# Kernel optimization log

Hardware: AMD Instinct MI355X
Metric: run time of the kernel (lower is better)

The kernel has to match this reference:

```python
import jax, jax.numpy as jnp
import numpy as np

N_CHEM = 200000
N_GENE = 20000
N_EDGES = 1000000
IN, HID, OUT = 128, 256, 128


def _seg_mean(msg, dst, num_segments):
    # DGL fn.mean: mean of incoming messages; nodes with zero in-degree get 0.
    s = jax.ops.segment_sum(msg, dst, num_segments=num_segments)
    cnt = jax.ops.segment_sum(jnp.ones((msg.shape[0],), msg.dtype), dst,
                              num_segments=num_segments)[:, None]
    return jnp.where(cnt > 0, s / jnp.maximum(cnt, 1.0), 0.0)


def setup_inputs() -> dict:
    key = jax.random.key(0)
    ks = jax.random.split(key, 12)
    d = {
        'src_cg': jax.random.randint(ks[0], (N_EDGES,), 0, N_CHEM, dtype=jnp.int32),
        'dst_cg': jax.random.randint(ks[1], (N_EDGES,), 0, N_GENE, dtype=jnp.int32),
        'src_gc': jax.random.randint(ks[2], (N_EDGES,), 0, N_GENE, dtype=jnp.int32),
        'dst_gc': jax.random.randint(ks[3], (N_EDGES,), 0, N_CHEM, dtype=jnp.int32),
        'embed_chem': jax.random.normal(ks[4], (N_CHEM, IN), jnp.float32) * 0.1,
        'embed_gene': jax.random.normal(ks[5], (N_GENE, IN), jnp.float32) * 0.1,
        'W1_cg': jax.random.normal(ks[6], (IN, HID), jnp.float32) * (1.0 / np.sqrt(IN)),
        'b1_cg': jnp.zeros((HID,), jnp.float32),
        'W1_gc': jax.random.normal(ks[7], (IN, HID), jnp.float32) * (1.0 / np.sqrt(IN)),
        'b1_gc': jnp.zeros((HID,), jnp.float32),
        'W2_cg': jax.random.normal(ks[8], (HID, OUT), jnp.float32) * (1.0 / np.sqrt(HID)),
        'b2_cg': jnp.zeros((OUT,), jnp.float32),
        'W2_gc': jax.random.normal(ks[9], (HID, OUT), jnp.float32) * (1.0 / np.sqrt(HID)),
        'b2_gc': jnp.zeros((OUT,), jnp.float32),
    }
    return d


def _layer(h_chem, h_gene, W_cg, b_cg, W_gc, b_gc, src_cg, dst_cg, src_gc, dst_gc):
    # per-etype linear transform on source features
    Wh_cg = h_chem @ W_cg + b_cg   # [N_CHEM, D]
    Wh_gc = h_gene @ W_gc + b_gc   # [N_GENE, D]
    # copy_u + mean per etype; multi_update_all('sum') -> single etype per dst here
    new_gene = _seg_mean(Wh_cg[src_cg], dst_cg, N_GENE)
    new_chem = _seg_mean(Wh_gc[src_gc], dst_gc, N_CHEM)
    return new_chem, new_gene


def reference(src_cg, dst_cg, src_gc, dst_gc, embed_chem, embed_gene,
              W1_cg, b1_cg, W1_gc, b1_gc, W2_cg, b2_cg, W2_gc, b2_gc):
    h_chem, h_gene = _layer(embed_chem, embed_gene, W1_cg, b1_cg, W1_gc, b1_gc,
                            src_cg, dst_cg, src_gc, dst_gc)
    h_chem = jax.nn.leaky_relu(h_chem, negative_slope=0.01)
    h_gene = jax.nn.leaky_relu(h_gene, negative_slope=0.01)
    h_chem, _ = _layer(h_chem, h_gene, W2_cg, b2_cg, W2_gc, b2_gc,
                       src_cg, dst_cg, src_gc, dst_gc)
    return h_chem  # [N_CHEM, OUT]
```

## Files before the change

kernel.cpp:

```cpp
#include <hip/hip_runtime.h>
#include <stdint.h>
#include <stddef.h>

#define N_CHEM 200000
#define N_GENE 20000
#define N_EDGES 1000000
#define IN_D 128
#define HID_D 256
#define OUT_D 128
#define N_SEG (N_GENE + N_CHEM)

#define NGB 313
#define NCB 391
#define NB  (NGB + NCB)
#define EPB 4096
#define NBA ((2 * N_EDGES + EPB - 1) / EPB)
#define NCONV 6250
#define NWT 16
#define CAP 8192
#define DROPPED 0x80000000

typedef float nfloat4 __attribute__((ext_vector_type(4)));
typedef __attribute__((ext_vector_type(8))) short bf16x8;
typedef __attribute__((ext_vector_type(4))) float f32x4;

__device__ inline unsigned bf16rne(float x) {
    unsigned u = __float_as_uint(x);
    return (u + 0x7FFFu + ((u >> 16) & 1u)) >> 16;
}

__device__ inline int bucket_of(int slot) {
    return (slot < N_GENE) ? (slot >> 6) : (NGB + ((slot - N_GENE) >> 9));
}
__device__ inline int bucket_slot0(int b) {
    return (b < NGB) ? (b << 6) : (N_GENE + ((b - NGB) << 9));
}


__global__ __launch_bounds__(256) void place_convert_kernel(
        const int* __restrict__ src_cg, const int* __restrict__ dst_cg,
        const int* __restrict__ src_gc, const int* __restrict__ dst_gc,
        int* __restrict__ bcur, unsigned* __restrict__ records,
        const float* __restrict__ conv_in, unsigned short* __restrict__ conv_out,
        const float* __restrict__ W1, const float* __restrict__ W2,
        unsigned short* __restrict__ W1t, unsigned short* __restrict__ W2t) {
    __shared__ unsigned stage_rec[EPB];
    __shared__ unsigned short stage_bkt[EPB];
    __shared__ int hist[NB];
    __shared__ int cursor[NB];
    __shared__ int tsum[256];
    const int tid = threadIdx.x;
    const int bid = blockIdx.x;

    if (bid >= NBA + NCONV) {
        unsigned short* tile = (unsigned short*)stage_rec;
        int wb = bid - NBA - NCONV;
        const float* Wsrc; unsigned short* Wdst; int K, N, kt0, n0;
        if (wb < 8) { Wsrc = W1; Wdst = W1t; K = 128; N = 256;
                      kt0 = (wb >> 2) * 64; n0 = (wb & 3) * 64; }
        else        { wb -= 8; Wsrc = W2; Wdst = W2t; K = 256; N = 128;
                      kt0 = (wb >> 1) * 64; n0 = (wb & 1) * 64; }
        #pragma unroll
        for (int it = 0; it < 16; ++it) {
            int idx = it * 256 + tid;
            int r = idx >> 6, c = idx & 63;
            tile[c * 65 + r] = (unsigned short)bf16rne(Wsrc[(size_t)(kt0 + r) * N + n0 + c]);
        }
        __syncthreads();
        #pragma unroll
        for (int it = 0; it < 16; ++it) {
            int idx = it * 256 + tid;
            int r = idx >> 6, c = idx & 63;
            Wdst[(size_t)(n0 + r) * K + kt0 + c] = tile[r * 65 + c];
        }
        return;
    }
    if (bid >= NBA) {
        int cb = bid - NBA;
        #pragma unroll
        for (int q = 0; q < 4; ++q) {
            int i = cb * 1024 + q * 256 + tid;
            if (i < N_CHEM * IN_D / 4) {
                float4 v = *(const float4*)&conv_in[(size_t)i * 4];
                uint2 w;
                w.x = bf16rne(v.x) | (bf16rne(v.y) << 16);
                w.y = bf16rne(v.z) | (bf16rne(v.w) << 16);
                *(uint2*)&conv_out[(size_t)i * 4] = w;
            }
        }
        return;
    }
    const int e0 = bid * EPB;
    const int cnt_blk = min(EPB, 2 * N_EDGES - e0);

    for (int i = tid; i < NB; i += 256) hist[i] = 0;
    __syncthreads();

    int slotR[EPB / 256], srcR[EPB / 256];
    #pragma unroll
    for (int q = 0; q < EPB / 256; ++q) {
        int e = e0 + q * 256 + tid;
        int slot = -1, s = 0;
        if (e < N_EDGES)            { slot = dst_cg[e];                    s = src_cg[e]; }
        else if (e < 2 * N_EDGES)   { slot = N_GENE + dst_gc[e - N_EDGES]; s = src_gc[e - N_EDGES]; }
        slotR[q] = slot; srcR[q] = s;
        if (slot >= 0) atomicAdd(&hist[bucket_of(slot)], 1);
    }
    __syncthreads();

    const int b3 = tid * 3;
    int h0 = (b3     < NB) ? hist[b3]     : 0;
    int h1 = (b3 + 1 < NB) ? hist[b3 + 1] : 0;
    int h2 = (b3 + 2 < NB) ? hist[b3 + 2] : 0;
    int ts = h0 + h1 + h2;
    tsum[tid] = ts;
    __syncthreads();
    for (int off = 1; off < 256; off <<= 1) {
        int t = (tid >= off) ? tsum[tid - off] : 0;
        __syncthreads();
        tsum[tid] += t;
        __syncthreads();
    }
    int base = tsum[tid] - ts;
    if (b3     < NB) cursor[b3]     = base;
    if (b3 + 1 < NB) cursor[b3 + 1] = base + h0;
    if (b3 + 2 < NB) cursor[b3 + 2] = base + h0 + h1;
    __syncthreads();

    #pragma unroll
    for (int q = 0; q < EPB / 256; ++q) {
        int slot = slotR[q];
        if (slot >= 0) {
            int b = bucket_of(slot);
            int p = atomicAdd(&cursor[b], 1);
            stage_rec[p] = ((unsigned)(slot - bucket_slot0(b)) << 18) | (unsigned)srcR[q];
            stage_bkt[p] = (unsigned short)b;
        }
    }
    __syncthreads();

    for (int i = tid; i < NB; i += 256) {
        int n = hist[i];
        if (n) {
            int got = atomicAdd(&bcur[i], n);
            int excl_i = cursor[i] - n;
            hist[i] = (got + n <= CAP) ? (i * CAP + got - excl_i) : (int)DROPPED;
        }
    }
    __syncthreads();

    for (int i = tid; i < cnt_blk; i += 256) {
        int d = hist[stage_bkt[i]];
        if (d != (int)DROPPED) records[i + d] = stage_rec[i];
    }
}


__global__ __launch_bounds__(256) void bin_b_kernel(
        const unsigned* __restrict__ records, const int* __restrict__ bcur,
        int* __restrict__ istart, int* __restrict__ iend, int* __restrict__ esrc) {
    __shared__ int hist[512];
    __shared__ int tsum[256];
    const int tid = threadIdx.x;
    const int b = blockIdx.x;
    int slot0 = bucket_slot0(b);
    int nslots = (b < NGB) ? min(64, N_GENE - slot0) : min(512, N_SEG - slot0);
    const int rbase = b * CAP;
    const int E = min(bcur[b], CAP);
    const unsigned* rec = &records[(size_t)b * CAP];

    hist[tid] = 0; hist[tid + 256] = 0;
    __syncthreads();
    for (int i = tid; i < E; i += 256)
        atomicAdd(&hist[rec[i] >> 18], 1);
    __syncthreads();

    int h0 = hist[2 * tid], h1 = hist[2 * tid + 1];
    int ts = h0 + h1;
    tsum[tid] = ts;
    __syncthreads();
    for (int off = 1; off < 256; off <<= 1) {
        int t = (tid >= off) ? tsum[tid - off] : 0;
        __syncthreads();
        tsum[tid] += t;
        __syncthreads();
    }
    int ex = tsum[tid] - ts;
    __syncthreads();
    hist[2 * tid]     = ex;
    hist[2 * tid + 1] = ex + h0;
    if (2 * tid < nslots) {
        istart[slot0 + 2 * tid] = rbase + ex;
        iend[slot0 + 2 * tid]   = rbase + ex + h0;
    }
    if (2 * tid + 1 < nslots) {
        istart[slot0 + 2 * tid + 1] = rbase + ex + h0;
        iend[slot0 + 2 * tid + 1]   = rbase + ex + h0 + h1;
    }
    __syncthreads();

    for (int i = tid; i < E; i += 256) {
        unsigned r = rec[i];
        int p = atomicAdd(&hist[r >> 18], 1);
        esrc[rbase + p] = (int)(r & 0x3FFFFu);
    }
}


__device__ inline void acc_u(float* a, uint4 v) {
    a[0] += __uint_as_float(v.x << 16); a[1] += __uint_as_float(v.x & 0xffff0000u);
    a[2] += __uint_as_float(v.y << 16); a[3] += __uint_as_float(v.y & 0xffff0000u);
    a[4] += __uint_as_float(v.z << 16); a[5] += __uint_as_float(v.z & 0xffff0000u);
    a[6] += __uint_as_float(v.w << 16); a[7] += __uint_as_float(v.w & 0xffff0000u);
}


__global__ __launch_bounds__(256) void gather_mean_bf16_split_kernel(
        const unsigned short* __restrict__ table,
        const int* __restrict__ istart, const int* __restrict__ iend,
        const int* __restrict__ esrc,
        unsigned short* __restrict__ outb, int n) {
    int lane = threadIdx.x & 15;
    int half = (threadIdx.x >> 4) & 1;
    int node = blockIdx.x * 8 + (threadIdx.x >> 5);
    if (node >= n) return;
    int s = istart[node], e = iend[node];
    int deg = e - s;
    int mid = s + ((deg + 1) >> 1);
    int j0 = half ? mid : s;
    int j1 = half ? e   : mid;
    int c = lane << 3;
    float acc[8] = {};
    int j = j0;
    for (; j + 8 <= j1; j += 8) {
        int i0 = esrc[j],     i1 = esrc[j + 1], i2 = esrc[j + 2], i3 = esrc[j + 3];
        int i4 = esrc[j + 4], i5 = esrc[j + 5], i6 = esrc[j + 6], i7 = esrc[j + 7];
        uint4 v0 = *(const uint4*)&table[(size_t)i0 * 128 + c];
        uint4 v1 = *(const uint4*)&table[(size_t)i1 * 128 + c];
        uint4 v2 = *(const uint4*)&table[(size_t)i2 * 128 + c];
        uint4 v3 = *(const uint4*)&table[(size_t)i3 * 128 + c];
        uint4 v4 = *(const uint4*)&table[(size_t)i4 * 128 + c];
        uint4 v5 = *(const uint4*)&table[(size_t)i5 * 128 + c];
        uint4 v6 = *(const uint4*)&table[(size_t)i6 * 128 + c];
        uint4 v7 = *(const uint4*)&table[(size_t)i7 * 128 + c];
        acc_u(acc, v0); acc_u(acc, v1); acc_u(acc, v2); acc_u(acc, v3);
        acc_u(acc, v4); acc_u(acc, v5); acc_u(acc, v6); acc_u(acc, v7);
    }
    for (; j + 4 <= j1; j += 4) {
        uint4 v0 = *(const uint4*)&table[(size_t)esrc[j]     * 128 + c];
        uint4 v1 = *(const uint4*)&table[(size_t)esrc[j + 1] * 128 + c];
        uint4 v2 = *(const uint4*)&table[(size_t)esrc[j + 2] * 128 + c];
        uint4 v3 = *(const uint4*)&table[(size_t)esrc[j + 3] * 128 + c];
        acc_u(acc, v0); acc_u(acc, v1); acc_u(acc, v2); acc_u(acc, v3);
    }
    for (; j < j1; ++j) {
        uint4 v = *(const uint4*)&table[(size_t)esrc[j] * 128 + c];
        acc_u(acc, v);
    }
    #pragma unroll
    for (int q = 0; q < 8; ++q) acc[q] += __shfl_xor(acc[q], 16);
    if (half == 0) {
        float inv = (deg > 0) ? 1.f / (float)deg : 0.f;
        #pragma unroll
        for (int q = 0; q < 8; ++q) acc[q] *= inv;
        uint4 w;
        w.x = bf16rne(acc[0]) | (bf16rne(acc[1]) << 16);
        w.y = bf16rne(acc[2]) | (bf16rne(acc[3]) << 16);
        w.z = bf16rne(acc[4]) | (bf16rne(acc[5]) << 16);
        w.w = bf16rne(acc[6]) | (bf16rne(acc[7]) << 16);
        *(uint4*)&outb[(size_t)node * 128 + c] = w;
    }
}


template<bool NT>
__global__ __launch_bounds__(256) void gather_mean_bf16_kernel(
        const unsigned short* __restrict__ table,
        const int* __restrict__ istart, const int* __restrict__ iend,
        const int* __restrict__ esrc,
        float* __restrict__ out, int n) {
    int lane = threadIdx.x & 15;
    int node = blockIdx.x * 16 + (threadIdx.x >> 4);
    if (node >= n) return;
    int s = istart[node], e = iend[node];
    int c = lane << 3;
    float acc[8] = {};
    int j = s;
    for (; j + 4 <= e; j += 4) {
        uint4 v0 = *(const uint4*)&table[(size_t)esrc[j]     * 128 + c];
        uint4 v1 = *(const uint4*)&table[(size_t)esrc[j + 1] * 128 + c];
        uint4 v2 = *(const uint4*)&table[(size_t)esrc[j + 2] * 128 + c];
        uint4 v3 = *(const uint4*)&table[(size_t)esrc[j + 3] * 128 + c];
        acc_u(acc, v0); acc_u(acc, v1); acc_u(acc, v2); acc_u(acc, v3);
    }
    for (; j < e; ++j) {
        uint4 v = *(const uint4*)&table[(size_t)esrc[j] * 128 + c];
        acc_u(acc, v);
    }
    int deg = e - s;
    float inv = (deg > 0) ? 1.f / (float)deg : 0.f;
    #pragma unroll
    for (int q = 0; q < 8; ++q) acc[q] *= inv;
    float* dst = &out[(size_t)node * 128 + c];
    if (NT) {
        nfloat4 a = { acc[0], acc[1], acc[2], acc[3] };
        nfloat4 b = { acc[4], acc[5], acc[6], acc[7] };
        __builtin_nontemporal_store(a, (nfloat4*)dst);
        __builtin_nontemporal_store(b, (nfloat4*)(dst + 4));
    } else {
        *(float4*)dst       = make_float4(acc[0], acc[1], acc[2], acc[3]);
        *(float4*)(dst + 4) = make_float4(acc[4], acc[5], acc[6], acc[7]);
    }
}


__global__ __launch_bounds__(256) void gather_mean_f32_kernel(
        const float* __restrict__ table,
        const int* __restrict__ istart, const int* __restrict__ iend,
        const int* __restrict__ esrc,
        float* __restrict__ out, int n) {
    int lane = threadIdx.x & 31;
    int node = blockIdx.x * 8 + (threadIdx.x >> 5);
    if (node >= n) return;
    int s = istart[node], e = iend[node];
    int c = lane << 2;
    float4 acc = make_float4(0.f, 0.f, 0.f, 0.f);
    int j = s;
    for (; j + 4 <= e; j += 4) {
        int s0 = esrc[j], s1 = esrc[j + 1], s2 = esrc[j + 2], s3 = esrc[j + 3];
        float4 v0 = *(const float4*)&table[(size_t)s0 * 128 + c];
        float4 v1 = *(const float4*)&table[(size_t)s1 * 128 + c];
        float4 v2 = *(const float4*)&table[(size_t)s2 * 128 + c];
        float4 v3 = *(const float4*)&table[(size_t)s3 * 128 + c];
        acc.x += (v0.x + v1.x) + (v2.x + v3.x);
        acc.y += (v0.y + v1.y) + (v2.y + v3.y);
        acc.z += (v0.z + v1.z) + (v2.z + v3.z);
        acc.w += (v0.w + v1.w) + (v2.w + v3.w);
    }
    for (; j < e; ++j) {
        float4 v = *(const float4*)&table[(size_t)esrc[j] * 128 + c];
        acc.x += v.x; acc.y += v.y; acc.z += v.z; acc.w += v.w;
    }
    int deg = e - s;
    float inv = (deg > 0) ? 1.f / (float)deg : 0.f;
    acc.x *= inv; acc.y *= inv; acc.z *= inv; acc.w *= inv;
    *(float4*)&out[(size_t)node * 128 + c] = acc;
}


template<int K, int N, bool MASK_LEAKY>
__global__ __launch_bounds__(256) void gemm_mfma_kernel(
        const unsigned short* __restrict__ A,
        const unsigned short* __restrict__ Wt,
        const float* __restrict__ bias,
        const int* __restrict__ istart, const int* __restrict__ iend,
        unsigned short* __restrict__ C,
        int M) {
    constexpr int BK  = 128;
    constexpr int LDK = BK + 8;
    __shared__ unsigned short As[64 * LDK];
    __shared__ unsigned short Ws[64 * LDK];
    const int tid  = threadIdx.x;
    const int lane = tid & 63;
    const int w    = tid >> 6;
    const int m0 = blockIdx.x * 64;
    const int n0 = blockIdx.y * 64;
    const int l15 = lane & 15;
    const int lhi = lane >> 4;
    f32x4 acc[4] = {};

    for (int kt0 = 0; kt0 < K; kt0 += BK) {
        #pragma unroll
        for (int it = 0; it < 4; ++it) {
            int idx = it * 256 + tid;
            int row = idx >> 4;
            int c8  = (idx & 15) << 3;
            uint4 v = make_uint4(0u, 0u, 0u, 0u);
            if (m0 + row < M)
                v = *(const uint4*)&A[(size_t)(m0 + row) * K + kt0 + c8];
            *(uint4*)&As[row * LDK + c8] = v;
        }
        #pragma unroll
        for (int it = 0; it < 4; ++it) {
            int idx = it * 256 + tid;
            int nrow = idx >> 4;
            int c8   = (idx & 15) << 3;
            uint4 v = *(const uint4*)&Wt[(size_t)(n0 + nrow) * K + kt0 + c8];
            *(uint4*)&Ws[nrow * LDK + c8] = v;
        }
        __syncthreads();

        #pragma unroll
        for (int kk = 0; kk < BK; kk += 32) {
            bf16x8 a = *(const bf16x8*)&As[(w * 16 + l15) * LDK + kk + lhi * 8];
            #pragma unroll
            for (int nt = 0; nt < 4; ++nt) {
                bf16x8 b = *(const bf16x8*)&Ws[(nt * 16 + l15) * LDK + kk + lhi * 8];
                acc[nt] = __builtin_amdgcn_mfma_f32_16x16x32_bf16(a, b, acc[nt], 0, 0, 0);
            }
        }
        __syncthreads();
    }

    #pragma unroll
    for (int nt = 0; nt < 4; ++nt) {
        int col = n0 + nt * 16 + l15;
        float bz = bias[col];
        #pragma unroll
        for (int r = 0; r < 4; ++r) {
            int row = m0 + w * 16 + lhi * 4 + r;
            if (row < M) {
                float v = acc[nt][r] + bz;
                if (MASK_LEAKY) {
                    int deg = iend[row] - istart[row];
                    v = (deg == 0) ? 0.f : (v > 0.f ? v : 0.01f * v);
                }
                C[(size_t)row * N + col] = (unsigned short)bf16rne(v);
            }
        }
    }
}


template<int K, int N, bool MASK_LEAKY, bool BF16_OUT>
__global__ __launch_bounds__(256) void gemm_kernel(const float* __restrict__ A,
                                                   const float* __restrict__ W,
                                                   const float* __restrict__ bias,
                                                   const int* __restrict__ istart,
                                                   const int* __restrict__ iend,
                                                   void* __restrict__ Cout, int M) {
    __shared__ float As[64 * 68];
    __shared__ float Ws[64 * 64];
    const int tid = threadIdx.x;
    const int tx = tid & 15, ty = tid >> 4;
    const int m0 = blockIdx.x * 64;
    const int n0 = blockIdx.y * 64;
    const int r0 = ty << 2, c0 = tx << 2;
    float acc[4][4] = {};

    for (int kt = 0; kt < K; kt += 64) {
        #pragma unroll
        for (int q = 0; q < 4; ++q) {
            int idx = tid + q * 256;
            int row = idx >> 4;
            int c4  = (idx & 15) << 2;
            float4 v = make_float4(0.f, 0.f, 0.f, 0.f);
            if (m0 + row < M)
                v = *(const float4*)&A[(size_t)(m0 + row) * K + kt + c4];
            *(float4*)&As[row * 68 + c4] = v;
        }
        #pragma unroll
        for (int q = 0; q < 4; ++q) {
            int idx = tid + q * 256;
            int k   = idx >> 4;
            int c4  = (idx & 15) << 2;
            *(float4*)&Ws[(k << 6) + c4] =
                *(const float4*)&W[(size_t)(kt + k) * N + n0 + c4];
        }
        __syncthreads();

        #pragma unroll 4
        for (int k = 0; k < 64; k += 4) {
            float a[4][4];
            #pragma unroll
            for (int r = 0; r < 4; ++r) {
                float4 v = *(const float4*)&As[(r0 + r) * 68 + k];
                a[r][0] = v.x; a[r][1] = v.y; a[r][2] = v.z; a[r][3] = v.w;
            }
            #pragma unroll
            for (int kk = 0; kk < 4; ++kk) {
                float4 w = *(const float4*)&Ws[((k + kk) << 6) + c0];
                #pragma unroll
                for (int r = 0; r < 4; ++r) {
                    acc[r][0] = fmaf(a[r][kk], w.x, acc[r][0]);
                    acc[r][1] = fmaf(a[r][kk], w.y, acc[r][1]);
                    acc[r][2] = fmaf(a[r][kk], w.z, acc[r][2]);
                    acc[r][3] = fmaf(a[r][kk], w.w, acc[r][3]);
                }
            }
        }
        __syncthreads();
    }

    float4 b = *(const float4*)&bias[n0 + c0];
    #pragma unroll
    for (int r = 0; r < 4; ++r) {
        int row = m0 + r0 + r;
        if (row < M) {
            float4 v;
            v.x = acc[r][0] + b.x; v.y = acc[r][1] + b.y;
            v.z = acc[r][2] + b.z; v.w = acc[r][3] + b.w;
            if (MASK_LEAKY) {
                int deg = iend[row] - istart[row];
                if (deg == 0) {
                    v = make_float4(0.f, 0.f, 0.f, 0.f);
                } else {
                    v.x = v.x > 0.f ? v.x : 0.01f * v.x;
                    v.y = v.y > 0.f ? v.y : 0.01f * v.y;
                    v.z = v.z > 0.f ? v.z : 0.01f * v.z;
                    v.w = v.w > 0.f ? v.w : 0.01f * v.w;
                }
            }
            if (BF16_OUT) {
                uint2 w;
                w.x = bf16rne(v.x) | (bf16rne(v.y) << 16);
                w.y = bf16rne(v.z) | (bf16rne(v.w) << 16);
                *(uint2*)&((unsigned short*)Cout)[(size_t)row * N + n0 + c0] = w;
            } else {
                *(float4*)&((float*)Cout)[(size_t)row * N + n0 + c0] = v;
            }
        }
    }
}


extern "C" void kernel_launch(void* const* d_in, const int* in_sizes, int n_in,
                              void* d_out, int out_size, void* d_ws, size_t ws_size,
                              hipStream_t stream) {
    const int*   src_cg     = (const int*)d_in[0];
    const int*   dst_cg     = (const int*)d_in[1];
    const int*   src_gc     = (const int*)d_in[2];
    const int*   dst_gc     = (const int*)d_in[3];
    const float* embed_chem = (const float*)d_in[4];
    const float* W1_cg = (const float*)d_in[6];
    const float* b1_cg = (const float*)d_in[7];
    const float* W2_gc = (const float*)d_in[12];
    const float* b2_gc = (const float*)d_in[13];
    float* out = (float*)d_out;

    int* ws_i = (int*)d_ws;
    size_t off = 0;
    int* bcur   = ws_i + off; off += NB;
    int* istart = ws_i + off; off += N_SEG;
    int* iend   = ws_i + off; off += N_SEG;
    off = (off + 3) & ~(size_t)3;
    int* esrc   = ws_i + off; off += (size_t)NB * CAP;
    size_t union_off = off;
    unsigned* records = (unsigned*)(ws_i + union_off);
    unsigned short* agg1b   = (unsigned short*)(ws_i + union_off);
    unsigned short* h_geneb = agg1b + (size_t)N_GENE * IN_D;
    float* agg1f   = (float*)(ws_i + union_off);
    float* h_genef = agg1f + (size_t)N_GENE * IN_D;
    size_t union_sz = (size_t)NB * CAP;
    if (union_sz < (size_t)N_GENE * (IN_D + HID_D)) union_sz = (size_t)N_GENE * (IN_D + HID_D);
    off = union_off + union_sz;
    unsigned short* Wh2b = (unsigned short*)(ws_i + off); off += (size_t)N_GENE * OUT_D / 2;
    unsigned short* embedb = (unsigned short*)(ws_i + off); off += (size_t)N_CHEM * IN_D / 2;
    unsigned short* W1t = (unsigned short*)(ws_i + off); off += (size_t)HID_D * IN_D / 2;
    unsigned short* W2t = (unsigned short*)(ws_i + off); off += (size_t)OUT_D * HID_D / 2;
    const bool bf16_embed = ws_size >= off * sizeof(int);

    (void)hipMemsetAsync(bcur, 0, NB * sizeof(int), stream);

    const int nextra = bf16_embed ? (NCONV + NWT) : 0;
    place_convert_kernel<<<NBA + nextra, 256, 0, stream>>>(
        src_cg, dst_cg, src_gc, dst_gc, bcur, records, embed_chem, embedb,
        W1_cg, W2_gc, W1t, W2t);
    bin_b_kernel<<<NB, 256, 0, stream>>>(records, bcur, istart, iend, esrc);

    if (bf16_embed) {
        gather_mean_bf16_split_kernel<<<(N_GENE + 7) / 8, 256, 0, stream>>>(
            embedb, istart, iend, esrc, agg1b, N_GENE);
        {
            dim3 g((N_GENE + 63) / 64, HID_D / 64), blk(256);
            gemm_mfma_kernel<IN_D, HID_D, true><<<g, blk, 0, stream>>>(
                agg1b, W1t, b1_cg, istart, iend, h_geneb, N_GENE);
        }
        {
            dim3 g((N_GENE + 63) / 64, OUT_D / 64), blk(256);
            gemm_mfma_kernel<HID_D, OUT_D, false><<<g, blk, 0, stream>>>(
                h_geneb, W2t, b2_gc, istart, iend, Wh2b, N_GENE);
        }
    } else {
        gather_mean_f32_kernel<<<(N_GENE + 7) / 8, 256, 0, stream>>>(
            embed_chem, istart, iend, esrc, agg1f, N_GENE);
        {
            dim3 g((N_GENE + 63) / 64, HID_D / 64), blk(256);
            gemm_kernel<IN_D, HID_D, true, false><<<g, blk, 0, stream>>>(
                agg1f, W1_cg, b1_cg, istart, iend, h_genef, N_GENE);
        }
        {
            dim3 g((N_GENE + 63) / 64, OUT_D / 64), blk(256);
            gemm_kernel<HID_D, OUT_D, false, true><<<g, blk, 0, stream>>>(
                h_genef, W2_gc, b2_gc, istart, iend, Wh2b, N_GENE);
        }
    }

    gather_mean_bf16_kernel<true><<<(N_CHEM + 15) / 16, 256, 0, stream>>>(
        Wh2b, istart + N_GENE, iend + N_GENE, esrc, out, N_CHEM);
}
```

Before: 331.3 us.

## Overlap chem-bucket binning with gene gather in a merged kernel

The second binning pass is split: gene buckets are binned first in a small launch, and chem-bucket binning runs inside the gene gather kernel as extra blocks. The two jobs touch disjoint data, so they can overlap and one launch's tail is hidden. The fallback f32 path keeps the original full binning. It relies on the gene and chem bucket regions of istart, iend and esrc being disjoint. Reads and writes now go through separate esrc pointers that alias the same buffer while both carry __restrict__.

```diff
diff --git a/kernel.cpp b/kernel.cpp
--- a/kernel.cpp
+++ b/kernel.cpp
@@ -17,6 +17,7 @@
 #define NBA ((2 * N_EDGES + EPB - 1) / EPB)
 #define NCONV 6250
 #define NWT 16
+#define NGGB ((N_GENE + 7) / 8)
 #define CAP 8192
 #define DROPPED 0x80000000
 
@@ -156,54 +157,60 @@
 }
 
 
+__device__ __forceinline__ void bin_b_body(
+        int b, const unsigned* __restrict__ records, const int* __restrict__ bcur,
+        int* __restrict__ istart, int* __restrict__ iend, int* __restrict__ esrc,
+        int* hist, int* tsum) {
+    const int tid = threadIdx.x;
+    int slot0 = bucket_slot0(b);
+    int nslots = (b < NGB) ? min(64, N_GENE - slot0) : min(512, N_SEG - slot0);
+    const int rbase = b * CAP;
+    const int E = min(bcur[b], CAP);
+    const unsigned* rec = &records[(size_t)b * CAP];
+
+    hist[tid] = 0; hist[tid + 256] = 0;
+    __syncthreads();
+    for (int i = tid; i < E; i += 256)
+        atomicAdd(&hist[rec[i] >> 18], 1);
+    __syncthreads();
+
+    int h0 = hist[2 * tid], h1 = hist[2 * tid + 1];
+    int ts = h0 + h1;
+    tsum[tid] = ts;
+    __syncthreads();
+    for (int off = 1; off < 256; off <<= 1) {
+        int t = (tid >= off) ? tsum[tid - off] : 0;
+        __syncthreads();
+        tsum[tid] += t;
+        __syncthreads();
+    }
+    int ex = tsum[tid] - ts;
+    __syncthreads();
+    hist[2 * tid]     = ex;
+    hist[2 * tid + 1] = ex + h0;
+    if (2 * tid < nslots) {
+        istart[slot0 + 2 * tid] = rbase + ex;
+        iend[slot0 + 2 * tid]   = rbase + ex + h0;
+    }
+    if (2 * tid + 1 < nslots) {
+        istart[slot0 + 2 * tid + 1] = rbase + ex + h0;
+        iend[slot0 + 2 * tid + 1]   = rbase + ex + h0 + h1;
+    }
+    __syncthreads();
+
+    for (int i = tid; i < E; i += 256) {
+        unsigned r = rec[i];
+        int p = atomicAdd(&hist[r >> 18], 1);
+        esrc[rbase + p] = (int)(r & 0x3FFFFu);
+    }
+}
+
 __global__ __launch_bounds__(256) void bin_b_kernel(
         const unsigned* __restrict__ records, const int* __restrict__ bcur,
         int* __restrict__ istart, int* __restrict__ iend, int* __restrict__ esrc) {
     __shared__ int hist[512];
     __shared__ int tsum[256];
-    const int tid = threadIdx.x;
-    const int b = blockIdx.x;
-    int slot0 = bucket_slot0(b);
-    int nslots = (b < NGB) ? min(64, N_GENE - slot0) : min(512, N_SEG - slot0);
-    const int rbase = b * CAP;
-    const int E = min(bcur[b], CAP);
-    const unsigned* rec = &records[(size_t)b * CAP];
-
-    hist[tid] = 0; hist[tid + 256] = 0;
-    __syncthreads();
-    for (int i = tid; i < E; i += 256)
-        atomicAdd(&hist[rec[i] >> 18], 1);
-    __syncthreads();
-
-    int h0 = hist[2 * tid], h1 = hist[2 * tid + 1];
-    int ts = h0 + h1;
-    tsum[tid] = ts;
-    __syncthreads();
-    for (int off = 1; off < 256; off <<= 1) {
-        int t = (tid >= off) ? tsum[tid - off] : 0;
-        __syncthreads();
-        tsum[tid] += t;
-        __syncthreads();
-    }
-    int ex = tsum[tid] - ts;
-    __syncthreads();
-    hist[2 * tid]     = ex;
-    hist[2 * tid + 1] = ex + h0;
-    if (2 * tid < nslots) {
-        istart[slot0 + 2 * tid] = rbase + ex;
-        iend[slot0 + 2 * tid]   = rbase + ex + h0;
-    }
-    if (2 * tid + 1 < nslots) {
-        istart[slot0 + 2 * tid + 1] = rbase + ex + h0;
-        iend[slot0 + 2 * tid + 1]   = rbase + ex + h0 + h1;
-    }
-    __syncthreads();
-
-    for (int i = tid; i < E; i += 256) {
-        unsigned r = rec[i];
-        int p = atomicAdd(&hist[r >> 18], 1);
-        esrc[rbase + p] = (int)(r & 0x3FFFFu);
-    }
+    bin_b_body(blockIdx.x, records, bcur, istart, iend, esrc, hist, tsum);
 }
 
 
@@ -215,14 +222,21 @@
 }
 
 
-__global__ __launch_bounds__(256) void gather_mean_bf16_split_kernel(
+__global__ __launch_bounds__(256) void gather_gene_chembin_kernel(
         const unsigned short* __restrict__ table,
-        const int* __restrict__ istart, const int* __restrict__ iend,
-        const int* __restrict__ esrc,
-        unsigned short* __restrict__ outb, int n) {
+        const int* __restrict__ esrc_ro,
+        unsigned short* __restrict__ outb, int n,
+        const unsigned* __restrict__ records, const int* __restrict__ bcur,
+        int* __restrict__ istart, int* __restrict__ iend, int* __restrict__ esrc_w) {
+    __shared__ int hist[512];
+    __shared__ int tsum[256];
+    if ((int)blockIdx.x < NCB) {
+        bin_b_body(NGB + blockIdx.x, records, bcur, istart, iend, esrc_w, hist, tsum);
+        return;
+    }
     int lane = threadIdx.x & 15;
     int half = (threadIdx.x >> 4) & 1;
-    int node = blockIdx.x * 8 + (threadIdx.x >> 5);
+    int node = (blockIdx.x - NCB) * 8 + (threadIdx.x >> 5);
     if (node >= n) return;
     int s = istart[node], e = iend[node];
     int deg = e - s;
@@ -233,8 +247,8 @@
     float acc[8] = {};
     int j = j0;
     for (; j + 8 <= j1; j += 8) {
-        int i0 = esrc[j],     i1 = esrc[j + 1], i2 = esrc[j + 2], i3 = esrc[j + 3];
-        int i4 = esrc[j + 4], i5 = esrc[j + 5], i6 = esrc[j + 6], i7 = esrc[j + 7];
+        int i0 = esrc_ro[j],     i1 = esrc_ro[j + 1], i2 = esrc_ro[j + 2], i3 = esrc_ro[j + 3];
+        int i4 = esrc_ro[j + 4], i5 = esrc_ro[j + 5], i6 = esrc_ro[j + 6], i7 = esrc_ro[j + 7];
         uint4 v0 = *(const uint4*)&table[(size_t)i0 * 128 + c];
         uint4 v1 = *(const uint4*)&table[(size_t)i1 * 128 + c];
         uint4 v2 = *(const uint4*)&table[(size_t)i2 * 128 + c];
@@ -247,14 +261,14 @@
         acc_u(acc, v4); acc_u(acc, v5); acc_u(acc, v6); acc_u(acc, v7);
     }
     for (; j + 4 <= j1; j += 4) {
-        uint4 v0 = *(const uint4*)&table[(size_t)esrc[j]     * 128 + c];
-        uint4 v1 = *(const uint4*)&table[(size_t)esrc[j + 1] * 128 + c];
-        uint4 v2 = *(const uint4*)&table[(size_t)esrc[j + 2] * 128 + c];
-        uint4 v3 = *(const uint4*)&table[(size_t)esrc[j + 3] * 128 + c];
+        uint4 v0 = *(const uint4*)&table[(size_t)esrc_ro[j]     * 128 + c];
+        uint4 v1 = *(const uint4*)&table[(size_t)esrc_ro[j + 1] * 128 + c];
+        uint4 v2 = *(const uint4*)&table[(size_t)esrc_ro[j + 2] * 128 + c];
+        uint4 v3 = *(const uint4*)&table[(size_t)esrc_ro[j + 3] * 128 + c];
         acc_u(acc, v0); acc_u(acc, v1); acc_u(acc, v2); acc_u(acc, v3);
     }
     for (; j < j1; ++j) {
-        uint4 v = *(const uint4*)&table[(size_t)esrc[j] * 128 + c];
+        uint4 v = *(const uint4*)&table[(size_t)esrc_ro[j] * 128 + c];
         acc_u(acc, v);
     }
     #pragma unroll
@@ -556,11 +570,11 @@
     place_convert_kernel<<<NBA + nextra, 256, 0, stream>>>(
         src_cg, dst_cg, src_gc, dst_gc, bcur, records, embed_chem, embedb,
         W1_cg, W2_gc, W1t, W2t);
-    bin_b_kernel<<<NB, 256, 0, stream>>>(records, bcur, istart, iend, esrc);
 
     if (bf16_embed) {
-        gather_mean_bf16_split_kernel<<<(N_GENE + 7) / 8, 256, 0, stream>>>(
-            embedb, istart, iend, esrc, agg1b, N_GENE);
+        bin_b_kernel<<<NGB, 256, 0, stream>>>(records, bcur, istart, iend, esrc);
+        gather_gene_chembin_kernel<<<NCB + NGGB, 256, 0, stream>>>(
+            embedb, esrc, agg1b, N_GENE, records, bcur, istart, iend, esrc);
         {
             dim3 g((N_GENE + 63) / 64, HID_D / 64), blk(256);
             gemm_mfma_kernel<IN_D, HID_D, true><<<g, blk, 0, stream>>>(
@@ -572,6 +586,7 @@
                 h_geneb, W2t, b2_gc, istart, iend, Wh2b, N_GENE);
         }
     } else {
+        bin_b_kernel<<<NB, 256, 0, stream>>>(records, bcur, istart, iend, esrc);
         gather_mean_f32_kernel<<<(N_GENE + 7) / 8, 256, 0, stream>>>(
             embed_chem, istart, iend, esrc, agg1f, N_GENE);
         {
```

Result: no change. 328.9 us (-0.7%).
